# Performance work log

Hardware: AMD Instinct MI355X
Metric: run time of the kernel (lower is better)

The kernel has to match this reference:

```python
import jax, jax.numpy as jnp
import numpy as np

TOP_K = 2
SCALING = 32.0 / 16.0  # lora_alpha / r

N, D, O = 4096, 4096, 4096   # tokens, in_features, out_features
E, H, R_RANK = 8, 3, 16      # experts, B-heads per expert, lora rank
W_SCALE = 0.02               # keep logits in a sane range


def setup_inputs() -> dict:
    key = jax.random.key(0)
    ks = jax.random.split(key, 6)
    return {
        "x": jax.random.normal(ks[0], (N, D), jnp.float32),
        "base_W": jax.random.normal(ks[1], (D, O), jnp.float32) * W_SCALE,
        "router_W": jax.random.normal(ks[2], (E, D), jnp.float32) * W_SCALE,
        "A": jax.random.normal(ks[3], (E, D, R_RANK), jnp.float32) * W_SCALE,
        "B": jax.random.normal(ks[4], (E, H, R_RANK, O), jnp.float32) * W_SCALE,
        "R": jax.random.normal(ks[5], (E, D, H), jnp.float32) * W_SCALE,
    }


def reference(x, base_W, router_W, A, B, R):
    # Base dense layer
    base = x @ base_W                                   # [N, O]
    # Expert router: softmax over experts, top-k gate renormalized
    probs = jax.nn.softmax(x @ router_W.T, axis=-1)     # [N, E]
    topv, topi = jax.lax.top_k(probs, TOP_K)            # [N, k]
    topv = topv / topv.sum(-1, keepdims=True)
    n_idx = jnp.arange(x.shape[0])[:, None]
    gate = jnp.zeros_like(probs).at[n_idx, topi].set(topv)  # dense [N, E] gate, 0 off top-k
    # Shared lora_A per expert
    a = jnp.einsum('nd,edr->ner', x, A)                 # [N, E, r]
    # Per-expert head router over lora_B heads
    head_w = jax.nn.softmax(jnp.einsum('nd,edh->neh', x, R), axis=-1)  # [N, E, H]
    # Head-weighted B projections, combined with expert gates
    delta = jnp.einsum('ner,neh,ehro,ne->no', a, head_w, B, gate)      # [N, O]
    return base + SCALING * delta
```

## Files before the change

### kernel.cpp

```cpp
#include <hip/hip_runtime.h>
#include <hip/hip_bf16.h>
#include <math.h>

typedef __bf16 bf16_t;
typedef __bf16 bf16x4_t __attribute__((ext_vector_type(4)));
typedef __bf16 bf16x8_t __attribute__((ext_vector_type(8)));
typedef float  f32x4_t  __attribute__((ext_vector_type(4)));

#define N_TOK 4096
#define D_IN  4096
#define O_OUT 4096
#define NEXP  8
#define NHEAD 3
#define RANK  16
#define KC2   384
#define XK    4480
#define PCOLS 256
#define NKZ   8
#define SCALING_F 2.0f


__device__ __forceinline__ void transpose_tile(const float* __restrict__ src,
                                               bf16_t* __restrict__ dst,
                                               int Rr, int Cc, int r0, int c0,
                                               float (*tile)[65]) {
  int q  = threadIdx.x & 15;
  int r4 = threadIdx.x >> 4;
  #pragma unroll
  for (int g = 0; g < 4; ++g) {
    int r = r4 + g * 16;
    float4 v = *(const float4*)(src + (size_t)(r0 + r) * Cc + c0 + q * 4);
    tile[r][q * 4 + 0] = v.x; tile[r][q * 4 + 1] = v.y;
    tile[r][q * 4 + 2] = v.z; tile[r][q * 4 + 3] = v.w;
  }
  __syncthreads();
  int j  = threadIdx.x & 7;
  int cc = threadIdx.x >> 3;
  #pragma unroll
  for (int h = 0; h < 2; ++h) {
    int c = cc + h * 32;
    bf16x8_t o;
    #pragma unroll
    for (int i = 0; i < 8; ++i) o[i] = (bf16_t)tile[j * 8 + i][c];
    *(bf16x8_t*)(dst + (size_t)(c0 + c) * Rr + r0 + j * 8) = o;
  }
}

__global__ __launch_bounds__(256) void prep_kernel(const float* __restrict__ x,
                                                   const float* __restrict__ base_W,
                                                   const float* __restrict__ rw,
                                                   const float* __restrict__ A,
                                                   const float* __restrict__ B,
                                                   const float* __restrict__ Rm,
                                                   bf16_t* __restrict__ xb2,
                                                   bf16_t* __restrict__ W2,
                                                   bf16_t* __restrict__ PabT,
                                                   int* __restrict__ gidx,
                                                   float* __restrict__ gwv) {
  __shared__ float tile[64][65];
  int b = blockIdx.x;
  if (b < 4096) {
    transpose_tile(base_W, W2, XK, 4096, (b & 63) * 64, (b >> 6) * 64, tile);
  } else if (b < 5120) {
    int lane = threadIdx.x & 63;
    int wv = threadIdx.x >> 6;
    int n = (b - 4096) * 4 + wv;
    const float4* xv = (const float4*)(x + (size_t)n * D_IN);
    bf16x4_t* xo = (bf16x4_t*)(xb2 + (size_t)n * XK);
    float acc[NEXP] = {0, 0, 0, 0, 0, 0, 0, 0};
    for (int d = lane; d < D_IN / 4; d += 64) {
      float4 xx = xv[d];
      bf16x4_t ob = { (bf16_t)xx.x, (bf16_t)xx.y, (bf16_t)xx.z, (bf16_t)xx.w };
      xo[d] = ob;
      #pragma unroll
      for (int e = 0; e < NEXP; ++e) {
        float4 ww = ((const float4*)(rw + (size_t)e * D_IN))[d];
        acc[e] += xx.x * ww.x + xx.y * ww.y + xx.z * ww.z + xx.w * ww.w;
      }
    }
    #pragma unroll
    for (int e = 0; e < NEXP; ++e) {
      float v = acc[e];
      #pragma unroll
      for (int o = 32; o > 0; o >>= 1) v += __shfl_down(v, o);
      acc[e] = v;
    }
    if (lane == 0) {
      int i0 = 0; float l0 = acc[0];
      #pragma unroll
      for (int e = 1; e < NEXP; ++e) if (acc[e] > l0) { l0 = acc[e]; i0 = e; }
      int i1 = -1; float l1 = -3.4e38f;
      #pragma unroll
      for (int e = 0; e < NEXP; ++e) if (e != i0 && acc[e] > l1) { l1 = acc[e]; i1 = e; }
      float w0 = 1.f / (1.f + expf(l1 - l0));
      gidx[2 * n] = i0; gidx[2 * n + 1] = i1;
      gwv[2 * n] = w0;  gwv[2 * n + 1] = 1.f - w0;
    }
  } else if (b < 5504) {
    int t = b - 5120;
    transpose_tile(B, W2 + 4096, XK, 4096, (t % 6) * 64, (t / 6) * 64, tile);
  } else {
    int c = b - 5504;
    for (int d = threadIdx.x; d < D_IN; d += 256) {
      float v = 0.f;
      if (c < 128) {
        int e = c >> 4, r = c & 15;
        v = A[((size_t)e * D_IN + d) * RANK + r];
      } else if (c < 152) {
        int qq = c - 128; int e = qq / 3, h = qq - 3 * e;
        v = Rm[((size_t)e * D_IN + d) * NHEAD + h];
      }
      PabT[(size_t)c * D_IN + d] = (bf16_t)v;
    }
  }
}

__global__ void gating_kernel(const float* __restrict__ projP, const int* __restrict__ gidx,
                              const float* __restrict__ gwv, bf16_t* __restrict__ xb2) {
  int n = blockIdx.x;
  int c = threadIdx.x;
  int e = c / 48;
  int h = (c % 48) / 16;
  int r = c & 15;
  int i0 = gidx[2 * n], i1 = gidx[2 * n + 1];
  float g = (e == i0) ? gwv[2 * n] : (e == i1) ? gwv[2 * n + 1] : 0.f;
  float val = 0.f;
  if (g != 0.f) {
    const float* p0 = projP + (size_t)n * PCOLS;
    const size_t S = (size_t)N_TOK * PCOLS;
    float h0 = 0.f, h1 = 0.f, h2 = 0.f, av = 0.f;
    #pragma unroll
    for (int z = 0; z < NKZ; ++z) {
      const float* pz = p0 + (size_t)z * S;
      h0 += pz[128 + e * 3 + 0];
      h1 += pz[128 + e * 3 + 1];
      h2 += pz[128 + e * 3 + 2];
      av += pz[e * 16 + r];
    }
    float mx = fmaxf(h0, fmaxf(h1, h2));
    float e0 = expf(h0 - mx), e1 = expf(h1 - mx), e2 = expf(h2 - mx);
    float hw = (h == 0 ? e0 : h == 1 ? e1 : e2) / (e0 + e1 + e2);
    val = SCALING_F * g * hw * av;
  }
  xb2[(size_t)n * XK + 4096 + c] = (bf16_t)val;
}

__device__ __forceinline__ void run_kloop(f32x4_t (&acc)[4][4], bf16_t* sA, bf16_t* sB,
                                          const bf16_t* __restrict__ Ab, int lda,
                                          const bf16_t* __restrict__ Bb, int ldb, int K) {
  const int tid = threadIdx.x;
  const int lane = tid & 63;
  const int w = tid >> 6;
  const int wm = (w >> 1) * 64;
  const int wn = (w & 1) * 64;
  const int qd = lane >> 4;
  const int ln = lane & 15;
  const int sw = ln & 7;

  size_t offA[4], offB[4];
  int lo[4];
  #pragma unroll
  for (int t = 0; t < 4; ++t) {
    int c = tid + t * 256;
    int m = c >> 3, kc = (c & 7) ^ (m & 7);
    offA[t] = (size_t)m * lda + kc * 8;
    offB[t] = (size_t)m * ldb + kc * 8;
    lo[t] = c * 8;
  }
  int rowA[4], rowB[4];
  #pragma unroll
  for (int i = 0; i < 4; ++i) {
    rowA[i] = (wm + i * 16 + ln) * 64;
    rowB[i] = (wn + i * 16 + ln) * 64;
  }

  for (int k0 = 0; k0 < K; k0 += 64) {
    __syncthreads();
    #pragma unroll
    for (int t = 0; t < 4; ++t)
      __builtin_amdgcn_global_load_lds(
          (const __attribute__((address_space(1))) void*)(Ab + k0 + offA[t]),
          (__attribute__((address_space(3))) void*)(sA + lo[t]), 16, 0, 0);
    #pragma unroll
    for (int t = 0; t < 4; ++t)
      __builtin_amdgcn_global_load_lds(
          (const __attribute__((address_space(1))) void*)(Bb + k0 + offB[t]),
          (__attribute__((address_space(3))) void*)(sB + lo[t]), 16, 0, 0);
    __syncthreads();
    #pragma unroll
    for (int s = 0; s < 2; ++s) {
      bf16x8_t af[4], bfr[4];
      int kx = ((s * 4 + qd) ^ sw) * 8;
      #pragma unroll
      for (int i = 0; i < 4; ++i) af[i]  = *(const bf16x8_t*)(sA + rowA[i] + kx);
      #pragma unroll
      for (int i = 0; i < 4; ++i) bfr[i] = *(const bf16x8_t*)(sB + rowB[i] + kx);
      #pragma unroll
      for (int i = 0; i < 4; ++i)
        #pragma unroll
        for (int j = 0; j < 4; ++j)
          acc[i][j] = __builtin_amdgcn_mfma_f32_16x16x32_bf16(af[i], bfr[j], acc[i][j], 0, 0, 0);
    }
  }
}

__global__ __launch_bounds__(256) void gemm_proj_kernel(const bf16_t* __restrict__ xb2,
                                                        const bf16_t* __restrict__ PabT,
                                                        float* __restrict__ projP) {
  __shared__ bf16_t sA[128 * 64];
  __shared__ bf16_t sB[128 * 64];
  int bm = blockIdx.x, bn = blockIdx.y, kz = blockIdx.z;
  f32x4_t acc[4][4] = {};
  run_kloop(acc, sA, sB,
            xb2 + (size_t)bm * 128 * XK + kz * 512, XK,
            PabT + (size_t)bn * 128 * D_IN + kz * 512, D_IN, 512);
  const int lane = threadIdx.x & 63, w = threadIdx.x >> 6;
  const int wm = (w >> 1) * 64, wn = (w & 1) * 64, qd = lane >> 4, ln = lane & 15;
  float* Cb = projP + (size_t)kz * N_TOK * PCOLS + (size_t)bm * 128 * PCOLS + bn * 128;
  #pragma unroll
  for (int i = 0; i < 4; ++i)
    #pragma unroll
    for (int j = 0; j < 4; ++j) {
      int col = wn + j * 16 + ln;
      #pragma unroll
      for (int rg = 0; rg < 4; ++rg) {
        int row = wm + i * 16 + qd * 4 + rg;
        Cb[(size_t)row * PCOLS + col] = acc[i][j][rg];
      }
    }
}


__device__ __forceinline__ void stage2(const bf16_t* __restrict__ G, int k0,
                                       bf16_t* lbase, size_t g0, size_t g1, int tid) {
  __builtin_amdgcn_global_load_lds(
      (const __attribute__((address_space(1))) void*)(G + g0 + k0),
      (__attribute__((address_space(3))) void*)(lbase + tid * 8), 16, 0, 0);
  __builtin_amdgcn_global_load_lds(
      (const __attribute__((address_space(1))) void*)(G + g1 + k0),
      (__attribute__((address_space(3))) void*)(lbase + 4096 + tid * 8), 16, 0, 0);
}

template <int N>
__device__ __forceinline__ void vm_wait() {
  if constexpr (N == 8)      asm volatile("s_waitcnt vmcnt(8)" ::: "memory");
  else if constexpr (N == 4) asm volatile("s_waitcnt vmcnt(4)" ::: "memory");
  else if constexpr (N == 0) asm volatile("s_waitcnt vmcnt(0)" ::: "memory");
}

template <int MB>
__device__ __forceinline__ void mfma16(f32x4_t (&acc)[8][4], const bf16x8_t (&af)[4],
                                       const bf16x8_t (&bv)[4]) {
  __builtin_amdgcn_s_setprio(1);
  #pragma unroll
  for (int mi = 0; mi < 4; ++mi)
    #pragma unroll
    for (int nj = 0; nj < 4; ++nj)
      acc[MB + mi][nj] =
          __builtin_amdgcn_mfma_f32_16x16x32_bf16(af[mi], bv[nj], acc[MB + mi][nj], 0, 0, 0);
  __builtin_amdgcn_s_setprio(0);
}

template <int SC, bool STAGE, int VMN, bool NEXTRD>
__device__ __forceinline__ void tbodyP(f32x4_t (&acc)[8][4], bf16_t* sring,
                                       const bf16_t* __restrict__ Ag,
                                       const bf16_t* __restrict__ Bg, int k3,
                                       size_t gA0, size_t gA1, size_t gB0, size_t gB1,
                                       int aoff, int boff, int tid,
                                       bf16x8_t (&bv)[4], bf16x8_t (&a0)[4]) {
  constexpr int SS = (SC + 3) & 3;
  constexpr int SN = (SC + 1) & 3;
  if constexpr (STAGE) stage2(Ag, k3, sring + SS * 16384, gA0, gA1, tid);
  const bf16_t* pA = sring + SC * 16384 + aoff;
  bf16x8_t a1[4];
  mfma16<0>(acc, a0, bv);
  #pragma unroll
  for (int mi = 0; mi < 4; ++mi) a1[mi] = *(const bf16x8_t*)(pA + (4 + mi) * 512);
  if constexpr (STAGE) stage2(Bg, k3, sring + SS * 16384 + 8192, gB0, gB1, tid);
  vm_wait<VMN>();
  __builtin_amdgcn_s_barrier();
  mfma16<4>(acc, a1, bv);
  if constexpr (NEXTRD) {
    const bf16_t* qA = sring + SN * 16384 + aoff;
    const bf16_t* qB = sring + SN * 16384 + 8192 + boff;
    #pragma unroll
    for (int nj = 0; nj < 4; ++nj) bv[nj] = *(const bf16x8_t*)(qB + nj * 512);
    #pragma unroll
    for (int mi = 0; mi < 4; ++mi) a0[mi] = *(const bf16x8_t*)(qA + mi * 512);
  }
  __builtin_amdgcn_sched_barrier(0);
  __builtin_amdgcn_s_barrier();
}

template <int K>
__device__ __forceinline__ void kloopP(f32x4_t (&acc)[8][4], bf16_t* sring,
                                       const bf16_t* __restrict__ A, int lda,
                                       const bf16_t* __restrict__ B, int ldb,
                                       int tid, int aoff, int boff) {
  constexpr int T = K / 32;
  static_assert((T & 3) == 0, "T must be multiple of 4");
  const int s0 = tid,       r0 = s0 >> 2, c0 = (s0 & 3) ^ ((r0 >> 1) & 3);
  const int s1 = 512 + tid, r1 = s1 >> 2, c1 = (s1 & 3) ^ ((r1 >> 1) & 3);
  const size_t gA0 = (size_t)r0 * lda + c0 * 8, gA1 = (size_t)r1 * lda + c1 * 8;
  const size_t gB0 = (size_t)r0 * ldb + c0 * 8, gB1 = (size_t)r1 * ldb + c1 * 8;

  #pragma unroll
  for (int t = 0; t < 3; ++t) {
    stage2(A, t * 32, sring + t * 16384, gA0, gA1, tid);
    stage2(B, t * 32, sring + t * 16384 + 8192, gB0, gB1, tid);
  }
  asm volatile("s_waitcnt vmcnt(8)" ::: "memory");
  __builtin_amdgcn_s_barrier();
  bf16x8_t bv[4], a0[4];
  {
    const bf16_t* qA = sring + aoff;
    const bf16_t* qB = sring + 8192 + boff;
    #pragma unroll
    for (int nj = 0; nj < 4; ++nj) bv[nj] = *(const bf16x8_t*)(qB + nj * 512);
    #pragma unroll
    for (int mi = 0; mi < 4; ++mi) a0[mi] = *(const bf16x8_t*)(qA + mi * 512);
  }
  constexpr int TM = T - 3;
  int t = 0;
  for (; t + 3 < TM; t += 4) {
    tbodyP<0,true,8,true>(acc, sring, A, B, (t+3)*32, gA0,gA1,gB0,gB1, aoff,boff,tid, bv,a0);
    tbodyP<1,true,8,true>(acc, sring, A, B, (t+4)*32, gA0,gA1,gB0,gB1, aoff,boff,tid, bv,a0);
    tbodyP<2,true,8,true>(acc, sring, A, B, (t+5)*32, gA0,gA1,gB0,gB1, aoff,boff,tid, bv,a0);
    tbodyP<3,true,8,true>(acc, sring, A, B, (t+6)*32, gA0,gA1,gB0,gB1, aoff,boff,tid, bv,a0);
  }
  tbodyP<0,true,8,true>(acc, sring, A, B, (t+3)*32, gA0,gA1,gB0,gB1, aoff,boff,tid, bv,a0);
  tbodyP<1,false,4,true >(acc, sring, A, B, 0, gA0,gA1,gB0,gB1, aoff,boff,tid, bv,a0);
  tbodyP<2,false,0,true >(acc, sring, A, B, 0, gA0,gA1,gB0,gB1, aoff,boff,tid, bv,a0);
  tbodyP<3,false,-1,false>(acc, sring, A, B, 0, gA0,gA1,gB0,gB1, aoff,boff,tid, bv,a0);
}

__global__ __launch_bounds__(512, 1) void gemm_fused256(const bf16_t* __restrict__ xb2,
                                                        const bf16_t* __restrict__ W2,
                                                        float* __restrict__ out) {
  __shared__ __align__(16) bf16_t sring[4 * 16384];
  const int tid = threadIdx.x;
  const int lane = tid & 63;
  const int w = tid >> 6;
  const int wm = w >> 2;
  const int wn = w & 3;
  const int qd = lane >> 4;
  const int ln = lane & 15;
  const int swz8 = ((qd ^ ((ln >> 1) & 3)) << 3);

  int b = blockIdx.x;
  int sw = (b & 7) * 32 + (b >> 3);
  int bm = sw >> 4, bn = sw & 15;

  const int aoff = (wm * 128 + ln) * 32 + swz8;
  const int boff = (wn * 64 + ln) * 32 + swz8;

  f32x4_t acc[8][4] = {};

  kloopP<XK>(acc, sring, xb2 + (size_t)bm * 256 * XK, XK,
                         W2  + (size_t)bn * 256 * XK, XK, tid, aoff, boff);

  float* Cb = out + (size_t)(bm * 256 + wm * 128) * O_OUT + bn * 256 + wn * 64;
  #pragma unroll
  for (int mi = 0; mi < 8; ++mi)
    #pragma unroll
    for (int nj = 0; nj < 4; ++nj)
      #pragma unroll
      for (int rg = 0; rg < 4; ++rg)
        Cb[(size_t)(mi * 16 + qd * 4 + rg) * O_OUT + nj * 16 + ln] = acc[mi][nj][rg];
}

extern "C" void kernel_launch(void* const* d_in, const int* in_sizes, int n_in,
                              void* d_out, int out_size, void* d_ws, size_t ws_size,
                              hipStream_t stream) {
  const float* x       = (const float*)d_in[0];
  const float* base_W  = (const float*)d_in[1];
  const float* routerW = (const float*)d_in[2];
  const float* A       = (const float*)d_in[3];
  const float* B       = (const float*)d_in[4];
  const float* Rm      = (const float*)d_in[5];
  float* out = (float*)d_out;
  char* ws = (char*)d_ws;

  bf16_t* xb2  = (bf16_t*)(ws);
  bf16_t* W2   = (bf16_t*)(ws + 36700160);
  bf16_t* PabT = (bf16_t*)(ws + 73400320);
  int*    gidx = (int*)   (ws + 75497472);
  float*  gwv  = (float*) (ws + 75530240);
  float*  projP = out;

  prep_kernel<<<5760, 256, 0, stream>>>(x, base_W, routerW, A, B, Rm,
                                        xb2, W2, PabT, gidx, gwv);
  gemm_proj_kernel<<<dim3(32, 2, NKZ), 256, 0, stream>>>(xb2, PabT, projP);
  gating_kernel<<<4096, 384, 0, stream>>>(projP, gidx, gwv, xb2);
  gemm_fused256<<<dim3(256), 512, 0, stream>>>(xb2, W2, out);
}
```

Before: 345.1 us.

## Double wavefronts per block in fused GEMM, halving per-wave N tile

The main 256x256 GEMM block now uses 1024 threads (16 waves in a 2x8 layout) instead of 512, so each wave computes a 128x32 sub-tile instead of 128x64. Each thread issues one global-to-LDS load per operand per stage instead of two, and the vmcnt waits are halved to match. The aim is more waves for latency hiding and fewer accumulator registers per wave. In exchange, each wave reads the same amount of A from LDS for half the MFMA work, which raises LDS traffic, and barriers now synchronize twice as many waves.

New measurement: 349.9 us (median of 2 runs). About the same (+1.4%).

```diff
diff --git a/kernel.cpp b/kernel.cpp
--- a/kernel.cpp
+++ b/kernel.cpp
@@ -231,60 +231,57 @@
 }
 
 
-__device__ __forceinline__ void stage2(const bf16_t* __restrict__ G, int k0,
-                                       bf16_t* lbase, size_t g0, size_t g1, int tid) {
+__device__ __forceinline__ void stage1(const bf16_t* __restrict__ G, int k0,
+                                       bf16_t* lbase, size_t g, int tid) {
   __builtin_amdgcn_global_load_lds(
-      (const __attribute__((address_space(1))) void*)(G + g0 + k0),
+      (const __attribute__((address_space(1))) void*)(G + g + k0),
       (__attribute__((address_space(3))) void*)(lbase + tid * 8), 16, 0, 0);
-  __builtin_amdgcn_global_load_lds(
-      (const __attribute__((address_space(1))) void*)(G + g1 + k0),
-      (__attribute__((address_space(3))) void*)(lbase + 4096 + tid * 8), 16, 0, 0);
 }
 
 template <int N>
 __device__ __forceinline__ void vm_wait() {
-  if constexpr (N == 8)      asm volatile("s_waitcnt vmcnt(8)" ::: "memory");
-  else if constexpr (N == 4) asm volatile("s_waitcnt vmcnt(4)" ::: "memory");
+  if constexpr (N == 4)      asm volatile("s_waitcnt vmcnt(4)" ::: "memory");
+  else if constexpr (N == 2) asm volatile("s_waitcnt vmcnt(2)" ::: "memory");
   else if constexpr (N == 0) asm volatile("s_waitcnt vmcnt(0)" ::: "memory");
 }
 
 template <int MB>
-__device__ __forceinline__ void mfma16(f32x4_t (&acc)[8][4], const bf16x8_t (&af)[4],
-                                       const bf16x8_t (&bv)[4]) {
+__device__ __forceinline__ void mfma8(f32x4_t (&acc)[8][2], const bf16x8_t (&af)[4],
+                                      const bf16x8_t (&bv)[2]) {
   __builtin_amdgcn_s_setprio(1);
   #pragma unroll
   for (int mi = 0; mi < 4; ++mi)
     #pragma unroll
-    for (int nj = 0; nj < 4; ++nj)
+    for (int nj = 0; nj < 2; ++nj)
       acc[MB + mi][nj] =
           __builtin_amdgcn_mfma_f32_16x16x32_bf16(af[mi], bv[nj], acc[MB + mi][nj], 0, 0, 0);
   __builtin_amdgcn_s_setprio(0);
 }
 
 template <int SC, bool STAGE, int VMN, bool NEXTRD>
-__device__ __forceinline__ void tbodyP(f32x4_t (&acc)[8][4], bf16_t* sring,
+__device__ __forceinline__ void tbodyP(f32x4_t (&acc)[8][2], bf16_t* sring,
                                        const bf16_t* __restrict__ Ag,
                                        const bf16_t* __restrict__ Bg, int k3,
-                                       size_t gA0, size_t gA1, size_t gB0, size_t gB1,
+                                       size_t gA, size_t gB,
                                        int aoff, int boff, int tid,
-                                       bf16x8_t (&bv)[4], bf16x8_t (&a0)[4]) {
+                                       bf16x8_t (&bv)[2], bf16x8_t (&a0)[4]) {
   constexpr int SS = (SC + 3) & 3;
   constexpr int SN = (SC + 1) & 3;
-  if constexpr (STAGE) stage2(Ag, k3, sring + SS * 16384, gA0, gA1, tid);
+  if constexpr (STAGE) stage1(Ag, k3, sring + SS * 16384, gA, tid);
   const bf16_t* pA = sring + SC * 16384 + aoff;
   bf16x8_t a1[4];
-  mfma16<0>(acc, a0, bv);
+  mfma8<0>(acc, a0, bv);
   #pragma unroll
   for (int mi = 0; mi < 4; ++mi) a1[mi] = *(const bf16x8_t*)(pA + (4 + mi) * 512);
-  if constexpr (STAGE) stage2(Bg, k3, sring + SS * 16384 + 8192, gB0, gB1, tid);
+  if constexpr (STAGE) stage1(Bg, k3, sring + SS * 16384 + 8192, gB, tid);
   vm_wait<VMN>();
   __builtin_amdgcn_s_barrier();
-  mfma16<4>(acc, a1, bv);
+  mfma8<4>(acc, a1, bv);
   if constexpr (NEXTRD) {
     const bf16_t* qA = sring + SN * 16384 + aoff;
     const bf16_t* qB = sring + SN * 16384 + 8192 + boff;
     #pragma unroll
-    for (int nj = 0; nj < 4; ++nj) bv[nj] = *(const bf16x8_t*)(qB + nj * 512);
+    for (int nj = 0; nj < 2; ++nj) bv[nj] = *(const bf16x8_t*)(qB + nj * 512);
     #pragma unroll
     for (int mi = 0; mi < 4; ++mi) a0[mi] = *(const bf16x8_t*)(qA + mi * 512);
   }
@@ -293,56 +290,55 @@
 }
 
 template <int K>
-__device__ __forceinline__ void kloopP(f32x4_t (&acc)[8][4], bf16_t* sring,
+__device__ __forceinline__ void kloopP(f32x4_t (&acc)[8][2], bf16_t* sring,
                                        const bf16_t* __restrict__ A, int lda,
                                        const bf16_t* __restrict__ B, int ldb,
                                        int tid, int aoff, int boff) {
   constexpr int T = K / 32;
   static_assert((T & 3) == 0, "T must be multiple of 4");
-  const int s0 = tid,       r0 = s0 >> 2, c0 = (s0 & 3) ^ ((r0 >> 1) & 3);
-  const int s1 = 512 + tid, r1 = s1 >> 2, c1 = (s1 & 3) ^ ((r1 >> 1) & 3);
-  const size_t gA0 = (size_t)r0 * lda + c0 * 8, gA1 = (size_t)r1 * lda + c1 * 8;
-  const size_t gB0 = (size_t)r0 * ldb + c0 * 8, gB1 = (size_t)r1 * ldb + c1 * 8;
+  const int s = tid, r = s >> 2, c = (s & 3) ^ ((r >> 1) & 3);
+  const size_t gA = (size_t)r * lda + c * 8;
+  const size_t gB = (size_t)r * ldb + c * 8;
 
   #pragma unroll
   for (int t = 0; t < 3; ++t) {
-    stage2(A, t * 32, sring + t * 16384, gA0, gA1, tid);
-    stage2(B, t * 32, sring + t * 16384 + 8192, gB0, gB1, tid);
-  }
-  asm volatile("s_waitcnt vmcnt(8)" ::: "memory");
+    stage1(A, t * 32, sring + t * 16384, gA, tid);
+    stage1(B, t * 32, sring + t * 16384 + 8192, gB, tid);
+  }
+  asm volatile("s_waitcnt vmcnt(4)" ::: "memory");
   __builtin_amdgcn_s_barrier();
-  bf16x8_t bv[4], a0[4];
+  bf16x8_t bv[2], a0[4];
   {
     const bf16_t* qA = sring + aoff;
     const bf16_t* qB = sring + 8192 + boff;
     #pragma unroll
-    for (int nj = 0; nj < 4; ++nj) bv[nj] = *(const bf16x8_t*)(qB + nj * 512);
+    for (int nj = 0; nj < 2; ++nj) bv[nj] = *(const bf16x8_t*)(qB + nj * 512);
     #pragma unroll
     for (int mi = 0; mi < 4; ++mi) a0[mi] = *(const bf16x8_t*)(qA + mi * 512);
   }
   constexpr int TM = T - 3;
   int t = 0;
   for (; t + 3 < TM; t += 4) {
-    tbodyP<0,true,8,true>(acc, sring, A, B, (t+3)*32, gA0,gA1,gB0,gB1, aoff,boff,tid, bv,a0);
-    tbodyP<1,true,8,true>(acc, sring, A, B, (t+4)*32, gA0,gA1,gB0,gB1, aoff,boff,tid, bv,a0);
-    tbodyP<2,true,8,true>(acc, sring, A, B, (t+5)*32, gA0,gA1,gB0,gB1, aoff,boff,tid, bv,a0);
-    tbodyP<3,true,8,true>(acc, sring, A, B, (t+6)*32, gA0,gA1,gB0,gB1, aoff,boff,tid, bv,a0);
-  }
-  tbodyP<0,true,8,true>(acc, sring, A, B, (t+3)*32, gA0,gA1,gB0,gB1, aoff,boff,tid, bv,a0);
-  tbodyP<1,false,4,true >(acc, sring, A, B, 0, gA0,gA1,gB0,gB1, aoff,boff,tid, bv,a0);
-  tbodyP<2,false,0,true >(acc, sring, A, B, 0, gA0,gA1,gB0,gB1, aoff,boff,tid, bv,a0);
-  tbodyP<3,false,-1,false>(acc, sring, A, B, 0, gA0,gA1,gB0,gB1, aoff,boff,tid, bv,a0);
-}
-
-__global__ __launch_bounds__(512, 1) void gemm_fused256(const bf16_t* __restrict__ xb2,
-                                                        const bf16_t* __restrict__ W2,
-                                                        float* __restrict__ out) {
+    tbodyP<0,true,4,true>(acc, sring, A, B, (t+3)*32, gA, gB, aoff, boff, tid, bv, a0);
+    tbodyP<1,true,4,true>(acc, sring, A, B, (t+4)*32, gA, gB, aoff, boff, tid, bv, a0);
+    tbodyP<2,true,4,true>(acc, sring, A, B, (t+5)*32, gA, gB, aoff, boff, tid, bv, a0);
+    tbodyP<3,true,4,true>(acc, sring, A, B, (t+6)*32, gA, gB, aoff, boff, tid, bv, a0);
+  }
+  tbodyP<0,true,4,true>(acc, sring, A, B, (t+3)*32, gA, gB, aoff, boff, tid, bv, a0);
+  tbodyP<1,false,2,true >(acc, sring, A, B, 0, gA, gB, aoff, boff, tid, bv, a0);
+  tbodyP<2,false,0,true >(acc, sring, A, B, 0, gA, gB, aoff, boff, tid, bv, a0);
+  tbodyP<3,false,-1,false>(acc, sring, A, B, 0, gA, gB, aoff, boff, tid, bv, a0);
+}
+
+__global__ __launch_bounds__(1024, 1) void gemm_fused256(const bf16_t* __restrict__ xb2,
+                                                         const bf16_t* __restrict__ W2,
+                                                         float* __restrict__ out) {
   __shared__ __align__(16) bf16_t sring[4 * 16384];
   const int tid = threadIdx.x;
   const int lane = tid & 63;
   const int w = tid >> 6;
-  const int wm = w >> 2;
-  const int wn = w & 3;
+  const int wm = w >> 3;
+  const int wn = w & 7;
   const int qd = lane >> 4;
   const int ln = lane & 15;
   const int swz8 = ((qd ^ ((ln >> 1) & 3)) << 3);
@@ -352,18 +348,18 @@
   int bm = sw >> 4, bn = sw & 15;
 
   const int aoff = (wm * 128 + ln) * 32 + swz8;
-  const int boff = (wn * 64 + ln) * 32 + swz8;
-
-  f32x4_t acc[8][4] = {};
+  const int boff = (wn * 32 + ln) * 32 + swz8;
+
+  f32x4_t acc[8][2] = {};
 
   kloopP<XK>(acc, sring, xb2 + (size_t)bm * 256 * XK, XK,
                          W2  + (size_t)bn * 256 * XK, XK, tid, aoff, boff);
 
-  float* Cb = out + (size_t)(bm * 256 + wm * 128) * O_OUT + bn * 256 + wn * 64;
+  float* Cb = out + (size_t)(bm * 256 + wm * 128) * O_OUT + bn * 256 + wn * 32;
   #pragma unroll
   for (int mi = 0; mi < 8; ++mi)
     #pragma unroll
-    for (int nj = 0; nj < 4; ++nj)
+    for (int nj = 0; nj < 2; ++nj)
       #pragma unroll
       for (int rg = 0; rg < 4; ++rg)
         Cb[(size_t)(mi * 16 + qd * 4 + rg) * O_OUT + nj * 16 + ln] = acc[mi][nj][rg];
@@ -392,5 +388,5 @@
                                         xb2, W2, PabT, gidx, gwv);
   gemm_proj_kernel<<<dim3(32, 2, NKZ), 256, 0, stream>>>(xb2, PabT, projP);
   gating_kernel<<<4096, 384, 0, stream>>>(projP, gidx, gwv, xb2);
-  gemm_fused256<<<dim3(256), 512, 0, stream>>>(xb2, W2, out);
-}
+  gemm_fused256<<<dim3(256), 1024, 0, stream>>>(xb2, W2, out);
+}
```
